# Kernel optimization log

Measured on AMD Instinct MI355X. Metric: run time of the kernel, lower is better.

Reference implementation:

```python
import jax, jax.numpy as jnp
import numpy as np

B, H, S, DK, DV = 2, 16, 2048, 64, 64


def setup_inputs() -> dict:
    key = jax.random.key(0)
    kq, kk, kv = jax.random.split(key, 3)
    queries = jax.random.normal(kq, (B, H, S, DK), dtype=jnp.float32)
    keys = jax.random.normal(kk, (B, H, S, DK), dtype=jnp.float32)
    values = jax.random.normal(kv, (B, H, S, DV), dtype=jnp.float32)
    # causal boolean mask, broadcastable over batch and heads
    mask = jnp.tril(jnp.ones((S, S), dtype=bool))[None, None, :, :]
    return {"queries": queries, "keys": keys, "values": values, "d_k": DK, "mask": mask}


def reference(queries, keys, values, d_k, mask):
    scale = 1.0 / jnp.sqrt(jnp.float32(d_k))
    # scores: [B, H, S, S]
    scores = jnp.einsum("bhqd,bhkd->bhqk", queries, keys) * scale
    mask_f = mask.astype(jnp.float32)
    scores = scores + (-1e9) * (1.0 - mask_f)
    weights = jax.nn.softmax(scores, axis=-1)
    # second mask step from the original: min(|mask|, |weights|)
    weights = jnp.minimum(jnp.abs(mask_f), jnp.abs(weights))
    return jnp.einsum("bhqk,bhkd->bhqd", weights, values)
```

## Files before the change

### kernel.cpp

```cpp
#include <hip/hip_runtime.h>
#include <hip/hip_bf16.h>

#define B_ 2
#define H_ 16
#define S_ 2048
#define D_ 64

typedef __attribute__((ext_vector_type(8))) short bf16x8;
typedef __attribute__((ext_vector_type(8))) unsigned short u16x8;
typedef __attribute__((ext_vector_type(4))) unsigned int u32x4;
typedef __attribute__((ext_vector_type(4))) float f32x4;
typedef unsigned short ushort_t;

#define SCALE 0.18033688011112042f
#define MFIX 12.0f

__device__ __forceinline__ unsigned short f2bf(float x) {
  unsigned int u = __builtin_bit_cast(unsigned int, x);
  unsigned int r = (u + 0x7FFFu + ((u >> 16) & 1u)) >> 16;
  return (unsigned short)r;
}

__device__ __forceinline__ unsigned int cvt_pk_bf16(float lo, float hi) {
  unsigned int r;
  asm("v_cvt_pk_bf16_f32 %0, %1, %2" : "=v"(r) : "v"(lo), "v"(hi));
  return r;
}

__device__ __forceinline__ float fast_exp2(float x) {
  float r;
  asm("v_exp_f32 %0, %1" : "=v"(r) : "v"(x));
  return r;
}

__device__ __forceinline__ int sigma_row(int rl) {
  return (rl & 0x23) | ((rl & 0x0C) << 1) | ((rl & 0x10) >> 2);
}

#define GLL16(gp, lp)                                                          \
  __builtin_amdgcn_global_load_lds(                                            \
      (const __attribute__((address_space(1))) unsigned int*)(gp),             \
      (__attribute__((address_space(3))) unsigned int*)(lp), 16, 0, 0)

__global__ void prepack(const float* __restrict__ Kf, const float* __restrict__ Vf,
                        ushort_t* __restrict__ Kg, ushort_t* __restrict__ Vtg) {
  const int blk = blockIdx.x;
  const int tid = threadIdx.x;
  const int bh = blk >> 5, t = blk & 31;
  const float* srcK = Kf + ((size_t)bh * S_ + (size_t)t * 64) * D_;
  const float* srcV = Vf + ((size_t)bh * S_ + (size_t)t * 64) * D_;
  ushort_t* dK = Kg + (size_t)blk * 4096;
  ushort_t* dV = Vtg + (size_t)blk * 4096;
  for (int is = 0; is < 2; ++is) {
    const int e = is * 2048 + tid * 8;
    {
      const int rl = e >> 6, pos = (e >> 3) & 7, ch = pos ^ (rl & 7);
      const float* sp = srcK + sigma_row(rl) * 64 + ch * 8;
      float4 a = *(const float4*)sp;
      float4 b = *(const float4*)(sp + 4);
      u16x8 w;
      w[0] = f2bf(a.x); w[1] = f2bf(a.y); w[2] = f2bf(a.z); w[3] = f2bf(a.w);
      w[4] = f2bf(b.x); w[5] = f2bf(b.y); w[6] = f2bf(b.z); w[7] = f2bf(b.w);
      *(u16x8*)(dK + e) = w;
    }
    {
      const int d0 = e >> 6, pos = (e >> 3) & 7, ch = pos ^ (d0 & 7);
      u16x8 w;
      for (int i = 0; i < 8; ++i) w[i] = f2bf(srcV[(size_t)(ch * 8 + i) * 64 + d0]);
      *(u16x8*)(dV + e) = w;
    }
  }
}

__launch_bounds__(512, 8)
__global__ void attn8w(const float* __restrict__ Qf, const ushort_t* __restrict__ Kg,
                       const ushort_t* __restrict__ Vtg, float* __restrict__ O,
                       float* __restrict__ PO, float* __restrict__ ML) {
  const int bh = blockIdx.x;
  const int y = blockIdx.y;
  int qb, c, t0, t1;
  if (y < 8) { qb = 8 + y; c = 0; t0 = 0; t1 = 15; }
  else {
    const int k = y - 8, pair = k >> 1;
    if ((k & 1) == 0) { qb = 15 - pair; c = 1; t0 = 16; t1 = 2 * qb + 1; }
    else              { qb = 7 - pair;  c = 0; t0 = 0;  t1 = 2 * qb + 1; }
  }

  const int tid = threadIdx.x;
  const int wave = tid >> 6, lane = tid & 63;
  const int col = lane & 15, g = lane >> 4;
  const int myqt = 2 * qb + (wave >> 2);
  const int qloc = (wave & 3) * 16 + col;

  __shared__ __align__(16) ushort_t Kl[2][64][64];
  __shared__ __align__(16) ushort_t Vt[2][64][64];

  const int qrow = qb * 128 + wave * 16 + col;
  bf16x8 qf[2];
  {
    const float* Qh = Qf + (size_t)bh * S_ * D_;
    for (int kk = 0; kk < 2; ++kk) {
      const float* p = Qh + (size_t)qrow * 64 + kk * 32 + g * 8;
      float4 a = *(const float4*)p;
      float4 b = *(const float4*)(p + 4);
      float v[8] = {a.x, a.y, a.z, a.w, b.x, b.y, b.z, b.w};
      bf16x8 w;
      for (int i = 0; i < 8; ++i) w[i] = (short)f2bf(v[i] * SCALE);
      qf[kk] = w;
    }
  }

  f32x4 acc[4] = {};
  float l_ = 0.0f;

  const int ch0 = (g ^ (col & 7)) << 3;
  const int ch1 = ((4 | g) ^ (col & 7)) << 3;

  auto STAGE = [&](int t, int b) {
    const ushort_t* kg = Kg + ((size_t)(bh * 32 + t)) * 4096;
    const ushort_t* vg = Vtg + ((size_t)(bh * 32 + t)) * 4096;
    GLL16(kg + tid * 8, &Kl[b][0][0] + tid * 8);
    GLL16(vg + tid * 8, &Vt[b][0][0] + tid * 8);
  };

  auto COMPUTE = [&](int b, bool diag) {
    const f32x4 cinit = {-MFIX, -MFIX, -MFIX, -MFIX};
    f32x4 s[4] = {cinit, cinit, cinit, cinit};
    __builtin_amdgcn_s_setprio(1);
    #pragma unroll
    for (int nt = 0; nt < 4; ++nt) {
      const ushort_t* row = &Kl[b][nt * 16 + col][0];
      const bf16x8 kf0 = *(const bf16x8*)(row + ch0);
      const bf16x8 kf1 = *(const bf16x8*)(row + ch1);
      s[nt] = __builtin_amdgcn_mfma_f32_16x16x32_bf16(kf0, qf[0], s[nt], 0, 0, 0);
      s[nt] = __builtin_amdgcn_mfma_f32_16x16x32_bf16(kf1, qf[1], s[nt], 0, 0, 0);
    }
    __builtin_amdgcn_s_setprio(0);
    if (diag) {
      #pragma unroll
      for (int nt = 0; nt < 4; ++nt) {
        const int tau_base = 32 * (nt >> 1) + 4 * (nt & 1) + 8 * g;
        #pragma unroll
        for (int r = 0; r < 4; ++r)
          if (tau_base + r > qloc) s[nt][r] = -INFINITY;
      }
    }
    #pragma unroll
    for (int nt = 0; nt < 4; ++nt)
      #pragma unroll
      for (int r = 0; r < 4; ++r) s[nt][r] = fast_exp2(s[nt][r]);
    const float b0 = (s[0][0] + s[0][1]) + (s[0][2] + s[0][3]);
    const float b1 = (s[1][0] + s[1][1]) + (s[1][2] + s[1][3]);
    const float b2 = (s[2][0] + s[2][1]) + (s[2][2] + s[2][3]);
    const float b3 = (s[3][0] + s[3][1]) + (s[3][2] + s[3][3]);
    l_ += (b0 + b1) + (b2 + b3);
    u32x4 w0, w1;
    w0[0] = cvt_pk_bf16(s[0][0], s[0][1]); w0[1] = cvt_pk_bf16(s[0][2], s[0][3]);
    w0[2] = cvt_pk_bf16(s[1][0], s[1][1]); w0[3] = cvt_pk_bf16(s[1][2], s[1][3]);
    w1[0] = cvt_pk_bf16(s[2][0], s[2][1]); w1[1] = cvt_pk_bf16(s[2][2], s[2][3]);
    w1[2] = cvt_pk_bf16(s[3][0], s[3][1]); w1[3] = cvt_pk_bf16(s[3][2], s[3][3]);
    const bf16x8 pf0 = __builtin_bit_cast(bf16x8, w0);
    const bf16x8 pf1 = __builtin_bit_cast(bf16x8, w1);
    __builtin_amdgcn_s_setprio(1);
    #pragma unroll
    for (int nt = 0; nt < 4; ++nt) {
      const ushort_t* row = &Vt[b][nt * 16 + col][0];
      const bf16x8 vf0 = *(const bf16x8*)(row + ch0);
      const bf16x8 vf1 = *(const bf16x8*)(row + ch1);
      acc[nt] = __builtin_amdgcn_mfma_f32_16x16x32_bf16(vf0, pf0, acc[nt], 0, 0, 0);
      acc[nt] = __builtin_amdgcn_mfma_f32_16x16x32_bf16(vf1, pf1, acc[nt], 0, 0, 0);
    }
    __builtin_amdgcn_s_setprio(0);
  };

  int cur = 0;
  STAGE(t0, 0);
  __syncthreads();
  for (int t = t0; t <= t1; ++t) {
    if (t < t1) STAGE(t + 1, cur ^ 1);
    if (t <= myqt) COMPUTE(cur, t == myqt);
    __syncthreads();
    cur ^= 1;
  }

  float lsum = l_;
  lsum += __shfl_xor(lsum, 16);
  lsum += __shfl_xor(lsum, 32);
  const int rowloc = wave * 16 + col;
  if (qb < 8) {
    const float inv = 1.0f / lsum;
    float* dst = O + (size_t)bh * S_ * D_ + (size_t)qrow * 64;
    #pragma unroll
    for (int nt = 0; nt < 4; ++nt) {
      f32x4 v = acc[nt];
      v *= inv;
      *(f32x4*)(dst + nt * 16 + 4 * g) = v;
    }
  } else {
    const int slot = ((bh << 3) + (qb - 8)) * 2 + c;
    float* po = PO + (size_t)slot * 8192;
    #pragma unroll
    for (int nt = 0; nt < 4; ++nt)
      *(f32x4*)(po + rowloc * 64 + nt * 16 + 4 * g) = acc[nt];
    if (g == 0) ML[(size_t)slot * 128 + rowloc] = lsum;
  }
}

__global__ void merge_partials(const float* __restrict__ PO, const float* __restrict__ ML,
                               float* __restrict__ O) {
  const int bh = blockIdx.x;
  const int q8 = blockIdx.y;
  const int tid = threadIdx.x;
  const int r = tid >> 2, d0 = (tid & 3) << 4;
  const int slot = ((bh << 3) + q8) * 2;
  const float l0 = ML[(size_t)slot * 128 + r];
  const float l1 = ML[(size_t)(slot + 1) * 128 + r];
  const float inv = 1.0f / (l0 + l1);
  const float* p0 = PO + (size_t)slot * 8192 + r * 64 + d0;
  const float* p1 = PO + (size_t)(slot + 1) * 8192 + r * 64 + d0;
  float* out = O + ((size_t)bh * S_ + (size_t)(8 + q8) * 128 + r) * 64 + d0;
  #pragma unroll
  for (int j = 0; j < 4; ++j) {
    float4 x = *(const float4*)(p0 + 4 * j);
    float4 yv = *(const float4*)(p1 + 4 * j);
    float4 o;
    o.x = (x.x + yv.x) * inv; o.y = (x.y + yv.y) * inv;
    o.z = (x.z + yv.z) * inv; o.w = (x.w + yv.w) * inv;
    *(float4*)(out + 4 * j) = o;
  }
}

__launch_bounds__(256, 4)
__global__ void attn_fb(const float* __restrict__ Qf, const float* __restrict__ Kf,
                        const float* __restrict__ Vf, float* __restrict__ O) {
  const int bh = blockIdx.x;
  const int qt = 31 - blockIdx.y;
  const int tid = threadIdx.x;
  const int wave = tid >> 6, lane = tid & 63;
  const int col = lane & 15, g = lane >> 4;
  __shared__ __align__(16) ushort_t Kl[2][64][64];
  __shared__ __align__(16) ushort_t Vt[2][64][64];
  const int qrow = qt * 64 + wave * 16 + col;
  bf16x8 qf[2];
  {
    const float* Qh = Qf + (size_t)bh * S_ * D_;
    for (int kk = 0; kk < 2; ++kk) {
      const float* pp = Qh + (size_t)qrow * 64 + kk * 32 + g * 8;
      float4 a = *(const float4*)pp;
      float4 b = *(const float4*)(pp + 4);
      float v[8] = {a.x, a.y, a.z, a.w, b.x, b.y, b.z, b.w};
      bf16x8 w;
      for (int i = 0; i < 8; ++i) w[i] = (short)f2bf(v[i] * SCALE);
      qf[kk] = w;
    }
  }
  f32x4 acc[4] = {};
  float l_ = 0.0f;
  const int ch0 = (g ^ (col & 7)) << 3;
  const int ch1 = ((4 | g) ^ (col & 7)) << 3;
  auto STAGE = [&](int t, int b) {
    const float* Kh = Kf + (size_t)bh * S_ * D_;
    const float* Vh = Vf + (size_t)bh * S_ * D_;
    {
      const int rl = tid >> 2;
      const int c0 = (tid & 3) << 4;
      const float* src = Kh + ((size_t)(t * 64 + sigma_row(rl))) * 64 + c0;
      for (int jj = 0; jj < 2; ++jj) {
        float4 x = *(const float4*)(src + jj * 8);
        float4 yv = *(const float4*)(src + jj * 8 + 4);
        u16x8 w;
        w[0] = f2bf(x.x); w[1] = f2bf(x.y); w[2] = f2bf(x.z); w[3] = f2bf(x.w);
        w[4] = f2bf(yv.x); w[5] = f2bf(yv.y); w[6] = f2bf(yv.z); w[7] = f2bf(yv.w);
        const int ch = (c0 >> 3) + jj;
        *(u16x8*)&Kl[b][rl][(ch ^ (rl & 7)) << 3] = w;
      }
    }
    {
      const int cc = tid & 63;
      const int r0 = (tid >> 6) << 4;
      const float* src = Vh + ((size_t)(t * 64 + r0)) * 64 + cc;
      for (int jj = 0; jj < 2; ++jj) {
        u16x8 w;
        for (int i = 0; i < 8; ++i) w[i] = f2bf(src[(size_t)(jj * 8 + i) * 64]);
        const int ch = (r0 >> 3) + jj;
        *(u16x8*)&Vt[b][cc][(ch ^ (cc & 7)) << 3] = w;
      }
    }
  };
  auto COMPUTE = [&](int b, bool diag) {
    const f32x4 cinit = {-MFIX, -MFIX, -MFIX, -MFIX};
    f32x4 s[4] = {cinit, cinit, cinit, cinit};
    for (int nt = 0; nt < 4; ++nt) {
      const ushort_t* row = &Kl[b][nt * 16 + col][0];
      const bf16x8 kf0 = *(const bf16x8*)(row + ch0);
      const bf16x8 kf1 = *(const bf16x8*)(row + ch1);
      s[nt] = __builtin_amdgcn_mfma_f32_16x16x32_bf16(kf0, qf[0], s[nt], 0, 0, 0);
      s[nt] = __builtin_amdgcn_mfma_f32_16x16x32_bf16(kf1, qf[1], s[nt], 0, 0, 0);
    }
    if (diag) {
      const int qloc = wave * 16 + col;
      for (int nt = 0; nt < 4; ++nt) {
        const int tb = 32 * (nt >> 1) + 4 * (nt & 1) + 8 * g;
        for (int r = 0; r < 4; ++r)
          if (tb + r > qloc) s[nt][r] = -INFINITY;
      }
    }
    float sum = 0.0f;
    for (int nt = 0; nt < 4; ++nt)
      for (int r = 0; r < 4; ++r) {
        const float pv = fast_exp2(s[nt][r]);
        s[nt][r] = pv;
        sum += pv;
      }
    l_ += sum;
    u32x4 t0, t1;
    t0[0] = cvt_pk_bf16(s[0][0], s[0][1]); t0[1] = cvt_pk_bf16(s[0][2], s[0][3]);
    t0[2] = cvt_pk_bf16(s[1][0], s[1][1]); t0[3] = cvt_pk_bf16(s[1][2], s[1][3]);
    t1[0] = cvt_pk_bf16(s[2][0], s[2][1]); t1[1] = cvt_pk_bf16(s[2][2], s[2][3]);
    t1[2] = cvt_pk_bf16(s[3][0], s[3][1]); t1[3] = cvt_pk_bf16(s[3][2], s[3][3]);
    const bf16x8 pf0 = __builtin_bit_cast(bf16x8, t0);
    const bf16x8 pf1 = __builtin_bit_cast(bf16x8, t1);
    for (int nt = 0; nt < 4; ++nt) {
      const ushort_t* row = &Vt[b][nt * 16 + col][0];
      const bf16x8 vf0 = *(const bf16x8*)(row + ch0);
      const bf16x8 vf1 = *(const bf16x8*)(row + ch1);
      acc[nt] = __builtin_amdgcn_mfma_f32_16x16x32_bf16(vf0, pf0, acc[nt], 0, 0, 0);
      acc[nt] = __builtin_amdgcn_mfma_f32_16x16x32_bf16(vf1, pf1, acc[nt], 0, 0, 0);
    }
  };
  int cur = 0;
  STAGE(0, 0);
  __syncthreads();
  for (int t = 0; t <= qt; ++t) {
    if (t < qt) STAGE(t + 1, cur ^ 1);
    COMPUTE(cur, t == qt);
    __syncthreads();
    cur ^= 1;
  }
  float lsum = l_;
  lsum += __shfl_xor(lsum, 16);
  lsum += __shfl_xor(lsum, 32);
  const float inv = 1.0f / lsum;
  float* dst = O + (size_t)bh * S_ * D_ + (size_t)qrow * 64;
  for (int nt = 0; nt < 4; ++nt) {
    f32x4 v = acc[nt];
    v *= inv;
    *(f32x4*)(dst + nt * 16 + 4 * g) = v;
  }
}

extern "C" void kernel_launch(void* const* d_in, const int* in_sizes, int n_in,
                              void* d_out, int out_size, void* d_ws, size_t ws_size,
                              hipStream_t stream) {
  const float* Q = (const float*)d_in[0];
  const float* K = (const float*)d_in[1];
  const float* V = (const float*)d_in[2];
  float* O = (float*)d_out;
  const size_t NE = (size_t)B_ * H_ * S_ * D_;
  const size_t needK = 2 * NE * sizeof(ushort_t);
  const size_t PO_elems = 32ull * 8 * 2 * 8192;
  const size_t ML_elems = 32ull * 8 * 2 * 128;
  const size_t needSplit = needK + (PO_elems + ML_elems) * sizeof(float);
  if (ws_size >= needSplit) {
    ushort_t* kg = (ushort_t*)d_ws;
    float* PO = (float*)((char*)d_ws + needK);
    float* ML = PO + PO_elems;
    prepack<<<1024, 256, 0, stream>>>(K, V, kg, kg + NE);
    attn8w<<<dim3(32, 24), 512, 0, stream>>>(Q, kg, kg + NE, O, PO, ML);
    merge_partials<<<dim3(32, 8), 512, 0, stream>>>(PO, ML, O);
  } else {
    attn_fb<<<dim3(32, 32), 256, 0, stream>>>(Q, K, V, O);
  }
}
```

Before: 50.95 us.

## Switch attention kernel to 32x32x16 MFMA with 4-wave blocks

Rewrites the main attention kernel to use 32x32x16 bf16 MFMA tiles instead of 16x16x32, with 4 waves of 32 query rows each rather than 8 waves of 16. The K prepack row permutation changes to match the new accumulator layout, and block-to-work mapping is reordered so blocks with y>=16 are mirrored. The aim is fewer MFMA issues and LDS fragment loads per tile, giving more reuse per LDS read. In exchange each thread holds more accumulator registers and there are fewer waves per block to hide latency.

```diff
diff --git a/kernel.cpp b/kernel.cpp
--- a/kernel.cpp
+++ b/kernel.cpp
@@ -9,6 +9,7 @@
 typedef __attribute__((ext_vector_type(8))) short bf16x8;
 typedef __attribute__((ext_vector_type(8))) unsigned short u16x8;
 typedef __attribute__((ext_vector_type(4))) unsigned int u32x4;
+typedef __attribute__((ext_vector_type(16))) float f32x16;
 typedef __attribute__((ext_vector_type(4))) float f32x4;
 typedef unsigned short ushort_t;
 
@@ -33,6 +34,9 @@
   return r;
 }
 
+__device__ __forceinline__ int sigma6(int rl) {
+  return (rl & 0x33) | ((rl & 4) << 1) | ((rl & 8) >> 1);
+}
 __device__ __forceinline__ int sigma_row(int rl) {
   return (rl & 0x23) | ((rl & 0x0C) << 1) | ((rl & 0x10) >> 2);
 }
@@ -55,7 +59,7 @@
     const int e = is * 2048 + tid * 8;
     {
       const int rl = e >> 6, pos = (e >> 3) & 7, ch = pos ^ (rl & 7);
-      const float* sp = srcK + sigma_row(rl) * 64 + ch * 8;
+      const float* sp = srcK + sigma6(rl) * 64 + ch * 8;
       float4 a = *(const float4*)sp;
       float4 b = *(const float4*)(sp + 4);
       u16x8 w;
@@ -72,12 +76,13 @@
   }
 }
 
-__launch_bounds__(512, 8)
-__global__ void attn8w(const float* __restrict__ Qf, const ushort_t* __restrict__ Kg,
+__launch_bounds__(256, 4)
+__global__ void attn32(const float* __restrict__ Qf, const ushort_t* __restrict__ Kg,
                        const ushort_t* __restrict__ Vtg, float* __restrict__ O,
                        float* __restrict__ PO, float* __restrict__ ML) {
   const int bh = blockIdx.x;
-  const int y = blockIdx.y;
+  int y = blockIdx.y;
+  if (y >= 16) y = 39 - y;
   int qb, c, t0, t1;
   if (y < 8) { qb = 8 + y; c = 0; t0 = 0; t1 = 15; }
   else {
@@ -87,89 +92,107 @@
   }
 
   const int tid = threadIdx.x;
-  const int wave = tid >> 6, lane = tid & 63;
-  const int col = lane & 15, g = lane >> 4;
-  const int myqt = 2 * qb + (wave >> 2);
-  const int qloc = (wave & 3) * 16 + col;
+  const int wq = tid >> 6, lane = tid & 63;
+  const int cq = lane & 31, hi = lane >> 5;
+  const int myqt = 2 * qb + (wq >> 1);
+  const int qloc64 = (wq & 1) * 32 + cq;
 
   __shared__ __align__(16) ushort_t Kl[2][64][64];
   __shared__ __align__(16) ushort_t Vt[2][64][64];
 
-  const int qrow = qb * 128 + wave * 16 + col;
-  bf16x8 qf[2];
+  const int qrow = qb * 128 + wq * 32 + cq;
+  bf16x8 qf[4];
   {
-    const float* Qh = Qf + (size_t)bh * S_ * D_;
-    for (int kk = 0; kk < 2; ++kk) {
-      const float* p = Qh + (size_t)qrow * 64 + kk * 32 + g * 8;
-      float4 a = *(const float4*)p;
-      float4 b = *(const float4*)(p + 4);
-      float v[8] = {a.x, a.y, a.z, a.w, b.x, b.y, b.z, b.w};
+    const float* qp = Qf + (size_t)bh * S_ * D_ + (size_t)qrow * D_ + 8 * hi;
+    #pragma unroll
+    for (int ks = 0; ks < 4; ++ks) {
+      float4 a = *(const float4*)(qp + ks * 16);
+      float4 b = *(const float4*)(qp + ks * 16 + 4);
       bf16x8 w;
-      for (int i = 0; i < 8; ++i) w[i] = (short)f2bf(v[i] * SCALE);
-      qf[kk] = w;
-    }
-  }
-
-  f32x4 acc[4] = {};
+      w[0] = (short)f2bf(a.x * SCALE); w[1] = (short)f2bf(a.y * SCALE);
+      w[2] = (short)f2bf(a.z * SCALE); w[3] = (short)f2bf(a.w * SCALE);
+      w[4] = (short)f2bf(b.x * SCALE); w[5] = (short)f2bf(b.y * SCALE);
+      w[6] = (short)f2bf(b.z * SCALE); w[7] = (short)f2bf(b.w * SCALE);
+      qf[ks] = w;
+    }
+  }
+
+  f32x16 acc0 = {}, acc1 = {};
   float l_ = 0.0f;
-
-  const int ch0 = (g ^ (col & 7)) << 3;
-  const int ch1 = ((4 | g) ^ (col & 7)) << 3;
+  const int xk = cq & 7;
 
   auto STAGE = [&](int t, int b) {
     const ushort_t* kg = Kg + ((size_t)(bh * 32 + t)) * 4096;
     const ushort_t* vg = Vtg + ((size_t)(bh * 32 + t)) * 4096;
-    GLL16(kg + tid * 8, &Kl[b][0][0] + tid * 8);
-    GLL16(vg + tid * 8, &Vt[b][0][0] + tid * 8);
+    GLL16(kg + tid * 8,        &Kl[b][0][0] + tid * 8);
+    GLL16(kg + 2048 + tid * 8, &Kl[b][0][0] + 2048 + tid * 8);
+    GLL16(vg + tid * 8,        &Vt[b][0][0] + tid * 8);
+    GLL16(vg + 2048 + tid * 8, &Vt[b][0][0] + 2048 + tid * 8);
   };
 
   auto COMPUTE = [&](int b, bool diag) {
-    const f32x4 cinit = {-MFIX, -MFIX, -MFIX, -MFIX};
-    f32x4 s[4] = {cinit, cinit, cinit, cinit};
+    const f32x16 cinit = {-MFIX, -MFIX, -MFIX, -MFIX, -MFIX, -MFIX, -MFIX, -MFIX,
+                          -MFIX, -MFIX, -MFIX, -MFIX, -MFIX, -MFIX, -MFIX, -MFIX};
+    f32x16 s0 = cinit, s1 = cinit;
+    const ushort_t* k0r = &Kl[b][cq][0];
+    const ushort_t* k1r = &Kl[b][32 + cq][0];
     __builtin_amdgcn_s_setprio(1);
     #pragma unroll
-    for (int nt = 0; nt < 4; ++nt) {
-      const ushort_t* row = &Kl[b][nt * 16 + col][0];
-      const bf16x8 kf0 = *(const bf16x8*)(row + ch0);
-      const bf16x8 kf1 = *(const bf16x8*)(row + ch1);
-      s[nt] = __builtin_amdgcn_mfma_f32_16x16x32_bf16(kf0, qf[0], s[nt], 0, 0, 0);
-      s[nt] = __builtin_amdgcn_mfma_f32_16x16x32_bf16(kf1, qf[1], s[nt], 0, 0, 0);
+    for (int ks = 0; ks < 4; ++ks) {
+      const int co = (((2 * ks + hi)) ^ xk) << 3;
+      const bf16x8 k0 = *(const bf16x8*)(k0r + co);
+      const bf16x8 k1 = *(const bf16x8*)(k1r + co);
+      s0 = __builtin_amdgcn_mfma_f32_32x32x16_bf16(k0, qf[ks], s0, 0, 0, 0);
+      s1 = __builtin_amdgcn_mfma_f32_32x32x16_bf16(k1, qf[ks], s1, 0, 0, 0);
     }
     __builtin_amdgcn_s_setprio(0);
     if (diag) {
       #pragma unroll
-      for (int nt = 0; nt < 4; ++nt) {
-        const int tau_base = 32 * (nt >> 1) + 4 * (nt & 1) + 8 * g;
-        #pragma unroll
-        for (int r = 0; r < 4; ++r)
-          if (tau_base + r > qloc) s[nt][r] = -INFINITY;
-      }
-    }
-    #pragma unroll
-    for (int nt = 0; nt < 4; ++nt)
-      #pragma unroll
-      for (int r = 0; r < 4; ++r) s[nt][r] = fast_exp2(s[nt][r]);
-    const float b0 = (s[0][0] + s[0][1]) + (s[0][2] + s[0][3]);
-    const float b1 = (s[1][0] + s[1][1]) + (s[1][2] + s[1][3]);
-    const float b2 = (s[2][0] + s[2][1]) + (s[2][2] + s[2][3]);
-    const float b3 = (s[3][0] + s[3][1]) + (s[3][2] + s[3][3]);
-    l_ += (b0 + b1) + (b2 + b3);
-    u32x4 w0, w1;
-    w0[0] = cvt_pk_bf16(s[0][0], s[0][1]); w0[1] = cvt_pk_bf16(s[0][2], s[0][3]);
-    w0[2] = cvt_pk_bf16(s[1][0], s[1][1]); w0[3] = cvt_pk_bf16(s[1][2], s[1][3]);
-    w1[0] = cvt_pk_bf16(s[2][0], s[2][1]); w1[1] = cvt_pk_bf16(s[2][2], s[2][3]);
-    w1[2] = cvt_pk_bf16(s[3][0], s[3][1]); w1[3] = cvt_pk_bf16(s[3][2], s[3][3]);
-    const bf16x8 pf0 = __builtin_bit_cast(bf16x8, w0);
-    const bf16x8 pf1 = __builtin_bit_cast(bf16x8, w1);
+      for (int r = 0; r < 16; ++r) {
+        const int tau = 16 * (r >> 3) + 4 * ((r >> 2) & 1) + (r & 3) + 8 * hi;
+        if (tau > qloc64) s0[r] = -INFINITY;
+        if (32 + tau > qloc64) s1[r] = -INFINITY;
+      }
+    }
+    #pragma unroll
+    for (int r = 0; r < 16; ++r) {
+      s0[r] = fast_exp2(s0[r]);
+      s1[r] = fast_exp2(s1[r]);
+    }
+    {
+      float a = (s0[0] + s0[1]) + (s0[2] + s0[3]);
+      float b2 = (s0[4] + s0[5]) + (s0[6] + s0[7]);
+      float c2 = (s0[8] + s0[9]) + (s0[10] + s0[11]);
+      float d2 = (s0[12] + s0[13]) + (s0[14] + s0[15]);
+      float e2 = (s1[0] + s1[1]) + (s1[2] + s1[3]);
+      float f2 = (s1[4] + s1[5]) + (s1[6] + s1[7]);
+      float g2 = (s1[8] + s1[9]) + (s1[10] + s1[11]);
+      float h2 = (s1[12] + s1[13]) + (s1[14] + s1[15]);
+      l_ += ((a + b2) + (c2 + d2)) + ((e2 + f2) + (g2 + h2));
+    }
+    unsigned W0[8], W1[8];
+    #pragma unroll
+    for (int j = 0; j < 8; ++j) {
+      W0[j] = cvt_pk_bf16(s0[2 * j], s0[2 * j + 1]);
+      W1[j] = cvt_pk_bf16(s1[2 * j], s1[2 * j + 1]);
+    }
+    const ushort_t* v0r = &Vt[b][cq][0];
+    const ushort_t* v1r = &Vt[b][32 + cq][0];
     __builtin_amdgcn_s_setprio(1);
-    #pragma unroll
-    for (int nt = 0; nt < 4; ++nt) {
-      const ushort_t* row = &Vt[b][nt * 16 + col][0];
-      const bf16x8 vf0 = *(const bf16x8*)(row + ch0);
-      const bf16x8 vf1 = *(const bf16x8*)(row + ch1);
-      acc[nt] = __builtin_amdgcn_mfma_f32_16x16x32_bf16(vf0, pf0, acc[nt], 0, 0, 0);
-      acc[nt] = __builtin_amdgcn_mfma_f32_16x16x32_bf16(vf1, pf1, acc[nt], 0, 0, 0);
-    }
+#define PVSTEP(ks, Wm)                                                         \
+    {                                                                          \
+      u32x4 t4;                                                                \
+      t4[0] = Wm[4 * ((ks) & 1) + 0]; t4[1] = Wm[4 * ((ks) & 1) + 1];          \
+      t4[2] = Wm[4 * ((ks) & 1) + 2]; t4[3] = Wm[4 * ((ks) & 1) + 3];          \
+      const bf16x8 pf = __builtin_bit_cast(bf16x8, t4);                        \
+      const int co = (((2 * (ks) + hi)) ^ xk) << 3;                            \
+      const bf16x8 a0 = *(const bf16x8*)(v0r + co);                            \
+      const bf16x8 a1 = *(const bf16x8*)(v1r + co);                            \
+      acc0 = __builtin_amdgcn_mfma_f32_32x32x16_bf16(a0, pf, acc0, 0, 0, 0);   \
+      acc1 = __builtin_amdgcn_mfma_f32_32x32x16_bf16(a1, pf, acc1, 0, 0, 0);   \
+    }
+    PVSTEP(0, W0) PVSTEP(1, W0) PVSTEP(2, W1) PVSTEP(3, W1)
+#undef PVSTEP
     __builtin_amdgcn_s_setprio(0);
   };
 
@@ -183,26 +206,37 @@
     cur ^= 1;
   }
 
-  float lsum = l_;
-  lsum += __shfl_xor(lsum, 16);
-  lsum += __shfl_xor(lsum, 32);
-  const int rowloc = wave * 16 + col;
+  float lsum = l_ + __shfl_xor(l_, 32);
+  const int rowloc = wq * 32 + cq;
   if (qb < 8) {
     const float inv = 1.0f / lsum;
     float* dst = O + (size_t)bh * S_ * D_ + (size_t)qrow * 64;
     #pragma unroll
-    for (int nt = 0; nt < 4; ++nt) {
-      f32x4 v = acc[nt];
-      v *= inv;
-      *(f32x4*)(dst + nt * 16 + 4 * g) = v;
+    for (int q2 = 0; q2 < 4; ++q2) {
+      f32x4 v0, v1;
+      #pragma unroll
+      for (int e = 0; e < 4; ++e) {
+        v0[e] = acc0[4 * q2 + e] * inv;
+        v1[e] = acc1[4 * q2 + e] * inv;
+      }
+      *(f32x4*)(dst + 8 * q2 + 4 * hi) = v0;
+      *(f32x4*)(dst + 32 + 8 * q2 + 4 * hi) = v1;
     }
   } else {
     const int slot = ((bh << 3) + (qb - 8)) * 2 + c;
-    float* po = PO + (size_t)slot * 8192;
-    #pragma unroll
-    for (int nt = 0; nt < 4; ++nt)
-      *(f32x4*)(po + rowloc * 64 + nt * 16 + 4 * g) = acc[nt];
-    if (g == 0) ML[(size_t)slot * 128 + rowloc] = lsum;
+    float* po = PO + (size_t)slot * 8192 + (size_t)rowloc * 64;
+    #pragma unroll
+    for (int q2 = 0; q2 < 4; ++q2) {
+      f32x4 v0, v1;
+      #pragma unroll
+      for (int e = 0; e < 4; ++e) {
+        v0[e] = acc0[4 * q2 + e];
+        v1[e] = acc1[4 * q2 + e];
+      }
+      *(f32x4*)(po + 8 * q2 + 4 * hi) = v0;
+      *(f32x4*)(po + 32 + 8 * q2 + 4 * hi) = v1;
+    }
+    if (hi == 0) ML[(size_t)slot * 128 + rowloc] = lsum;
   }
 }
 
@@ -366,7 +400,7 @@
     float* PO = (float*)((char*)d_ws + needK);
     float* ML = PO + PO_elems;
     prepack<<<1024, 256, 0, stream>>>(K, V, kg, kg + NE);
-    attn8w<<<dim3(32, 24), 512, 0, stream>>>(Q, kg, kg + NE, O, PO, ML);
+    attn32<<<dim3(32, 24), 256, 0, stream>>>(Q, kg, kg + NE, O, PO, ML);
     merge_partials<<<dim3(32, 8), 512, 0, stream>>>(PO, ML, O);
   } else {
     attn_fb<<<dim3(32, 32), 256, 0, stream>>>(Q, K, V, O);
```

New measurement: 51.60 us. Within noise of the previous version (+1.3%).

## Drop LDS staging; load prepacked K/V MFMA fragments directly from global

Applied to the files above, without the earlier changes.

The prepack kernel now writes K and transposed V in per-lane MFMA fragment order, so each wave can load its operands straight from global memory into registers. The attention kernel no longer uses shared memory or double-buffered global-to-LDS copies, removes the per-tile __syncthreads, and lets each wave stop at its own causal end tile. This targets barrier and LDS traffic costs. In exchange, every wave re-reads the same K/V tile from global/L2 with no software prefetch overlap, and the occupancy hint drops from 8 to 4.

```diff
diff --git a/kernel.cpp b/kernel.cpp
--- a/kernel.cpp
+++ b/kernel.cpp
@@ -36,11 +36,6 @@
 __device__ __forceinline__ int sigma_row(int rl) {
   return (rl & 0x23) | ((rl & 0x0C) << 1) | ((rl & 0x10) >> 2);
 }
-
-#define GLL16(gp, lp)                                                          \
-  __builtin_amdgcn_global_load_lds(                                            \
-      (const __attribute__((address_space(1))) unsigned int*)(gp),             \
-      (__attribute__((address_space(3))) unsigned int*)(lp), 16, 0, 0)
 
 __global__ void prepack(const float* __restrict__ Kf, const float* __restrict__ Vf,
                         ushort_t* __restrict__ Kg, ushort_t* __restrict__ Vtg) {
@@ -53,9 +48,12 @@
   ushort_t* dV = Vtg + (size_t)blk * 4096;
   for (int is = 0; is < 2; ++is) {
     const int e = is * 2048 + tid * 8;
+    const int frag = e >> 9;
+    const int l = (e >> 3) & 63;
+    const int nt = frag >> 1, kk = frag & 1;
+    const int colx = l & 15, gx = l >> 4;
     {
-      const int rl = e >> 6, pos = (e >> 3) & 7, ch = pos ^ (rl & 7);
-      const float* sp = srcK + sigma_row(rl) * 64 + ch * 8;
+      const float* sp = srcK + (size_t)sigma_row(nt * 16 + colx) * 64 + kk * 32 + gx * 8;
       float4 a = *(const float4*)sp;
       float4 b = *(const float4*)(sp + 4);
       u16x8 w;
@@ -64,18 +62,18 @@
       *(u16x8*)(dK + e) = w;
     }
     {
-      const int d0 = e >> 6, pos = (e >> 3) & 7, ch = pos ^ (d0 & 7);
+      const float* spv = srcV + (size_t)(kk * 32 + gx * 8) * 64 + nt * 16 + colx;
       u16x8 w;
-      for (int i = 0; i < 8; ++i) w[i] = f2bf(srcV[(size_t)(ch * 8 + i) * 64 + d0]);
+      for (int i = 0; i < 8; ++i) w[i] = f2bf(spv[(size_t)i * 64]);
       *(u16x8*)(dV + e) = w;
     }
   }
 }
 
-__launch_bounds__(512, 8)
-__global__ void attn8w(const float* __restrict__ Qf, const ushort_t* __restrict__ Kg,
-                       const ushort_t* __restrict__ Vtg, float* __restrict__ O,
-                       float* __restrict__ PO, float* __restrict__ ML) {
+__launch_bounds__(512, 4)
+__global__ void attn_nl(const float* __restrict__ Qf, const ushort_t* __restrict__ Kg,
+                        const ushort_t* __restrict__ Vtg, float* __restrict__ O,
+                        float* __restrict__ PO, float* __restrict__ ML) {
   const int bh = blockIdx.x;
   const int y = blockIdx.y;
   int qb, c, t0, t1;
@@ -91,9 +89,7 @@
   const int col = lane & 15, g = lane >> 4;
   const int myqt = 2 * qb + (wave >> 2);
   const int qloc = (wave & 3) * 16 + col;
-
-  __shared__ __align__(16) ushort_t Kl[2][64][64];
-  __shared__ __align__(16) ushort_t Vt[2][64][64];
+  const int tEnd = (myqt < t1) ? myqt : t1;
 
   const int qrow = qb * 128 + wave * 16 + col;
   bf16x8 qf[2];
@@ -113,30 +109,28 @@
   f32x4 acc[4] = {};
   float l_ = 0.0f;
 
-  const int ch0 = (g ^ (col & 7)) << 3;
-  const int ch1 = ((4 | g) ^ (col & 7)) << 3;
-
-  auto STAGE = [&](int t, int b) {
-    const ushort_t* kg = Kg + ((size_t)(bh * 32 + t)) * 4096;
-    const ushort_t* vg = Vtg + ((size_t)(bh * 32 + t)) * 4096;
-    GLL16(kg + tid * 8, &Kl[b][0][0] + tid * 8);
-    GLL16(vg + tid * 8, &Vt[b][0][0] + tid * 8);
-  };
-
-  auto COMPUTE = [&](int b, bool diag) {
+  const ushort_t* kbase = Kg + ((size_t)(bh * 32)) * 4096 + (size_t)lane * 8;
+  const ushort_t* vbase = Vtg + ((size_t)(bh * 32)) * 4096 + (size_t)lane * 8;
+
+  for (int t = t0; t <= tEnd; ++t) {
+    const ushort_t* kb = kbase + (size_t)t * 4096;
+    const ushort_t* vb = vbase + (size_t)t * 4096;
+    bf16x8 kr[8];
+    #pragma unroll
+    for (int f = 0; f < 8; ++f) kr[f] = *(const bf16x8*)(kb + f * 512);
     const f32x4 cinit = {-MFIX, -MFIX, -MFIX, -MFIX};
     f32x4 s[4] = {cinit, cinit, cinit, cinit};
     __builtin_amdgcn_s_setprio(1);
     #pragma unroll
     for (int nt = 0; nt < 4; ++nt) {
-      const ushort_t* row = &Kl[b][nt * 16 + col][0];
-      const bf16x8 kf0 = *(const bf16x8*)(row + ch0);
-      const bf16x8 kf1 = *(const bf16x8*)(row + ch1);
-      s[nt] = __builtin_amdgcn_mfma_f32_16x16x32_bf16(kf0, qf[0], s[nt], 0, 0, 0);
-      s[nt] = __builtin_amdgcn_mfma_f32_16x16x32_bf16(kf1, qf[1], s[nt], 0, 0, 0);
+      s[nt] = __builtin_amdgcn_mfma_f32_16x16x32_bf16(kr[2 * nt], qf[0], s[nt], 0, 0, 0);
+      s[nt] = __builtin_amdgcn_mfma_f32_16x16x32_bf16(kr[2 * nt + 1], qf[1], s[nt], 0, 0, 0);
     }
     __builtin_amdgcn_s_setprio(0);
-    if (diag) {
+    bf16x8 vr[8];
+    #pragma unroll
+    for (int f = 0; f < 8; ++f) vr[f] = *(const bf16x8*)(vb + f * 512);
+    if (t == myqt) {
       #pragma unroll
       for (int nt = 0; nt < 4; ++nt) {
         const int tau_base = 32 * (nt >> 1) + 4 * (nt & 1) + 8 * g;
@@ -164,23 +158,10 @@
     __builtin_amdgcn_s_setprio(1);
     #pragma unroll
     for (int nt = 0; nt < 4; ++nt) {
-      const ushort_t* row = &Vt[b][nt * 16 + col][0];
-      const bf16x8 vf0 = *(const bf16x8*)(row + ch0);
-      const bf16x8 vf1 = *(const bf16x8*)(row + ch1);
-      acc[nt] = __builtin_amdgcn_mfma_f32_16x16x32_bf16(vf0, pf0, acc[nt], 0, 0, 0);
-      acc[nt] = __builtin_amdgcn_mfma_f32_16x16x32_bf16(vf1, pf1, acc[nt], 0, 0, 0);
+      acc[nt] = __builtin_amdgcn_mfma_f32_16x16x32_bf16(vr[2 * nt], pf0, acc[nt], 0, 0, 0);
+      acc[nt] = __builtin_amdgcn_mfma_f32_16x16x32_bf16(vr[2 * nt + 1], pf1, acc[nt], 0, 0, 0);
     }
     __builtin_amdgcn_s_setprio(0);
-  };
-
-  int cur = 0;
-  STAGE(t0, 0);
-  __syncthreads();
-  for (int t = t0; t <= t1; ++t) {
-    if (t < t1) STAGE(t + 1, cur ^ 1);
-    if (t <= myqt) COMPUTE(cur, t == myqt);
-    __syncthreads();
-    cur ^= 1;
   }
 
   float lsum = l_;
@@ -366,7 +347,7 @@
     float* PO = (float*)((char*)d_ws + needK);
     float* ML = PO + PO_elems;
     prepack<<<1024, 256, 0, stream>>>(K, V, kg, kg + NE);
-    attn8w<<<dim3(32, 24), 512, 0, stream>>>(Q, kg, kg + NE, O, PO, ML);
+    attn_nl<<<dim3(32, 24), 512, 0, stream>>>(Q, kg, kg + NE, O, PO, ML);
     merge_partials<<<dim3(32, 8), 512, 0, stream>>>(PO, ML, O);
   } else {
     attn_fb<<<dim3(32, 32), 256, 0, stream>>>(Q, K, V, O);
```

Result: slower. 64.35 us (+26.3%).
